# Performance work log

Hardware: AMD Instinct MI355X
Metric: run time of the kernel (lower is better)

Reference implementation:

```python
import jax, jax.numpy as jnp
import numpy as np

B, T, HID = 8, 1024, 2048
H, D = 16, 128          # num_attention_heads, head_dim (num_kv_heads = 1)
Q_RANK, KV_RANK = 128, 64
EPS = 1e-6
MIN_VAL = -1e9          # fp32 branch of create_causal_padding_mask


def _rmsnorm(x, w, eps=EPS):
    return x * jax.lax.rsqrt(jnp.mean(x * x, axis=-1, keepdims=True) + eps) * w


def _rope(x, cos, sin):
    x1, x2 = jnp.split(x, 2, axis=-1)
    return jnp.concatenate([x1 * cos - x2 * sin, x2 * cos + x1 * sin], axis=-1)


def setup_inputs() -> dict:
    key = jax.random.key(0)
    ks = jax.random.split(key, 12)
    s = lambda fan_in: 1.0 / np.sqrt(fan_in)
    return {
        'hidden_states': jax.random.normal(ks[0], (B, T, HID), jnp.float32),
        'cos_g': jax.random.uniform(ks[1], (1, T, 1, D // 2), jnp.float32, -1.0, 1.0),
        'sin_g': jax.random.uniform(ks[2], (1, T, 1, D // 2), jnp.float32, -1.0, 1.0),
        'cos_l': jax.random.uniform(ks[3], (1, T, 1, D // 2), jnp.float32, -1.0, 1.0),
        'sin_l': jax.random.uniform(ks[4], (1, T, 1, D // 2), jnp.float32, -1.0, 1.0),
        'Wq_a': jax.random.normal(ks[5], (HID, Q_RANK), jnp.float32) * s(HID),
        'bq_a': jnp.zeros((Q_RANK,), jnp.float32),
        'Wq_b': jax.random.normal(ks[6], (Q_RANK, H * D), jnp.float32) * s(Q_RANK),
        'bq_b': jnp.zeros((H * D,), jnp.float32),
        'Wkv_a': jax.random.normal(ks[7], (HID, KV_RANK), jnp.float32) * s(HID),
        'bkv_a': jnp.zeros((KV_RANK,), jnp.float32),
        'Wkv_b': jax.random.normal(ks[8], (KV_RANK, 2 * D), jnp.float32) * s(KV_RANK),
        'bkv_b': jnp.zeros((2 * D,), jnp.float32),
        'q_norm_w': jnp.ones((D,), jnp.float32),
        'kv_norm_w': jnp.ones((KV_RANK,), jnp.float32),
        'Wo': jax.random.normal(ks[9], (H * D, HID), jnp.float32) * s(H * D),
        'nope_logit': jnp.array([-2.0], jnp.float32),
        'gl_logit': jnp.array([np.log(0.01 / 0.99)], jnp.float32),
        'attention_mask': jnp.ones((B, T), jnp.int32),
    }


def reference(hidden_states, cos_g, sin_g, cos_l, sin_l,
              Wq_a, bq_a, Wq_b, bq_b, Wkv_a, bkv_a, Wkv_b, bkv_b,
              q_norm_w, kv_norm_w, Wo, nope_logit, gl_logit, attention_mask):
    h = hidden_states
    # learned global/local RoPE blend
    a = jax.nn.sigmoid(gl_logit).reshape(1, 1, 1, 1)
    cos = cos_g * a + cos_l * (1.0 - a)
    sin = sin_g * a + sin_l * (1.0 - a)

    # LoRA q path: q_b(RMSNorm(q_a(h)))
    q = _rmsnorm(h @ Wq_a + bq_a, q_norm_w) @ Wq_b + bq_b      # [B,T,H*D]
    q = q.reshape(B, T, H, D)
    q_pe = _rope(q, cos, sin)

    # LoRA kv path: kv_b(RMSNorm(kv_a(h)))  (single kv head)
    kv = _rmsnorm(h @ Wkv_a + bkv_a, kv_norm_w) @ Wkv_b + bkv_b  # [B,T,2*D]
    k, v = jnp.split(kv, 2, axis=-1)                            # [B,T,D] each
    k_pe = _rope(k.reshape(B, T, 1, D), cos, sin)[:, :, 0, :]   # [B,T,D]

    # nope/rope alpha mix
    na = jax.nn.sigmoid(nope_logit).reshape(1, 1, 1, 1)
    q_f = na * q + (1.0 - na) * q_pe                            # [B,T,H,D]
    k_f = na[..., 0] * k + (1.0 - na[..., 0]) * k_pe            # [B,T,D]

    # causal + padding additive mask
    causal = jnp.triu(jnp.ones((T, T), bool), k=1)              # [T,T]
    pad = (attention_mask == 0)[:, None, None, :]               # [B,1,1,T]
    add_mask = jnp.where(causal[None, None] | pad, MIN_VAL, 0.0).astype(h.dtype)

    scale = D ** -0.5
    scores = jnp.einsum('bthd,bsd->bhts', q_f, k_f) * scale + add_mask
    attn = jax.nn.softmax(scores, axis=-1)                      # [B,H,T,T]
    out = jnp.einsum('bhts,bsd->bthd', attn, v)                 # [B,T,H,D]
    return out.reshape(B, T, H * D) @ Wo
```

## Files before the change

### kernel.cpp

```cpp
#include <hip/hip_runtime.h>
#include <hip/hip_bf16.h>

typedef __attribute__((ext_vector_type(8))) short bf16x8;
typedef __attribute__((ext_vector_type(4))) float f32x4;
typedef __attribute__((ext_vector_type(4))) unsigned short us4;

#define DEV __device__ __forceinline__

constexpr int Bc = 8, Tc = 1024, HIDc = 2048, Hc = 16, Dc = 128;
constexpr int ROWSc = Bc * Tc;

DEV unsigned short f2bfb(float x) {
  union { float f; unsigned u; } v; v.f = x;
  unsigned r = v.u + 0x7fffu + ((v.u >> 16) & 1u);
  return (unsigned short)(r >> 16);
}
DEV float bfb2f(unsigned short b) {
  union { unsigned u; float f; } v; v.u = ((unsigned)b) << 16; return v.f;
}
DEV float fexp2(float x) { return __builtin_amdgcn_exp2f(x); }
DEV unsigned pkbf(float lo, float hi) {
  union { float f; unsigned u; } a, b; a.f = lo; b.f = hi;
  return ((b.u + 0x8000u) & 0xffff0000u) | ((a.u + 0x8000u) >> 16);
}

DEV void gload16(const void* g, void* l) {
  __builtin_amdgcn_global_load_lds(
      (const __attribute__((address_space(1))) unsigned int*)g,
      (__attribute__((address_space(3))) unsigned int*)l, 16, 0, 0);
}


__global__ void k_blend(const float* __restrict__ cg, const float* __restrict__ sg,
                        const float* __restrict__ cl, const float* __restrict__ sl,
                        const float* __restrict__ gl,
                        float* __restrict__ cosb, float* __restrict__ sinb) {
  int u = blockIdx.x * 256 + threadIdx.x;
  if (u >= Tc * 64) return;
  float a = 1.0f / (1.0f + __expf(-gl[0]));
  cosb[u] = cg[u] * a + cl[u] * (1.0f - a);
  sinb[u] = sg[u] * a + sl[u] * (1.0f - a);
}

__global__ void k_zero(unsigned short* __restrict__ p, int n) {
  int i = blockIdx.x * 256 + threadIdx.x;
  if (i < n) p[i] = 0;
}

__global__ __launch_bounds__(256) void k_transpose(const float* __restrict__ in,
                                                   unsigned short* __restrict__ out,
                                                   int R, int C) {
  __shared__ float tile[32][33];
  int tx = threadIdx.x & 31, ty = threadIdx.x >> 5;
  int r0 = blockIdx.y * 32, c0 = blockIdx.x * 32;
#pragma unroll
  for (int i = 0; i < 4; i++)
    tile[ty + i * 8][tx] = in[(size_t)(r0 + ty + i * 8) * C + c0 + tx];
  __syncthreads();
#pragma unroll
  for (int i = 0; i < 4; i++) {
    int rr = ty + i * 8;
    out[(size_t)(c0 + rr) * R + r0 + tx] = f2bfb(tile[tx][rr]);
  }
}


__global__ __launch_bounds__(256) void k_gemm1(const float* __restrict__ A,
                                               const unsigned short* __restrict__ Bt,
                                               float* __restrict__ C) {
  constexpr int K = 2048, N = 256;
  __shared__ __align__(16) unsigned short As[64 * 32];
  __shared__ __align__(16) unsigned short Bs[128 * 32];
  int lin = blockIdx.x;
  int wg = (lin & 7) * 32 + (lin >> 3);
  int m0 = (wg >> 1) * 64, n0 = (wg & 1) * 128;
  int tid = threadIdx.x, lane = tid & 63, wc = tid >> 6;
  int ar = tid >> 2, akc = (tid & 3) * 8;
  const float* Ag = A + (size_t)(m0 + ar) * K + akc;
  const unsigned short* Bg0 = Bt + (size_t)(n0 + ar) * K + akc;
  const unsigned short* Bg1 = Bt + (size_t)(n0 + 64 + ar) * K + akc;
  unsigned short* Bsl0 = &Bs[tid * 8];
  unsigned short* Bsl1 = &Bs[2048 + tid * 8];
  f32x4 acc[4][2];
  f32x4 zz = {0.f, 0.f, 0.f, 0.f};
#pragma unroll
  for (int m = 0; m < 4; m++)
#pragma unroll
    for (int n = 0; n < 2; n++) acc[m][n] = zz;
  int fr = lane & 15, fk = (lane >> 4) * 8;
  for (int kt = 0; kt < K; kt += 32) {
    float4 a0 = *(const float4*)(Ag + kt);
    float4 a1 = *(const float4*)(Ag + kt + 4);
    __syncthreads();
    gload16(Bg0 + kt, Bsl0);
    gload16(Bg1 + kt, Bsl1);
    us4 c0 = { f2bfb(a0.x), f2bfb(a0.y), f2bfb(a0.z), f2bfb(a0.w) };
    us4 c1 = { f2bfb(a1.x), f2bfb(a1.y), f2bfb(a1.z), f2bfb(a1.w) };
    *(us4*)&As[ar * 32 + akc] = c0;
    *(us4*)&As[ar * 32 + akc + 4] = c1;
    __syncthreads();
    bf16x8 af[4], bfv[2];
#pragma unroll
    for (int i = 0; i < 4; i++)
      af[i] = *(const bf16x8*)&As[(i * 16 + fr) * 32 + fk];
#pragma unroll
    for (int i = 0; i < 2; i++)
      bfv[i] = *(const bf16x8*)&Bs[(wc * 32 + i * 16 + fr) * 32 + fk];
    __builtin_amdgcn_s_setprio(1);
#pragma unroll
    for (int m = 0; m < 4; m++)
#pragma unroll
      for (int n = 0; n < 2; n++)
        acc[m][n] = __builtin_amdgcn_mfma_f32_16x16x32_bf16(af[m], bfv[n], acc[m][n], 0, 0, 0);
    __builtin_amdgcn_s_setprio(0);
  }
  int gg = lane >> 4;
#pragma unroll
  for (int m = 0; m < 4; m++)
#pragma unroll
    for (int n = 0; n < 2; n++)
#pragma unroll
      for (int r = 0; r < 4; r++) {
        size_t row = (size_t)m0 + m * 16 + gg * 4 + r;
        size_t col = (size_t)n0 + wc * 32 + n * 16 + fr;
        C[row * N + col] = acc[m][n][r];
      }
}


template <int OUTB>
__global__ __launch_bounds__(256) void k_gemm(const unsigned short* __restrict__ A,
                                              const unsigned short* __restrict__ Bt,
                                              void* __restrict__ outp,
                                              int M, int N, int K, int nx) {
  __shared__ __align__(16) unsigned short As[4096];
  __shared__ __align__(16) unsigned short Bs[4096];
  int lin = blockIdx.x;
  int qq = gridDim.x >> 3;
  int wg = (lin & 7) * qq + (lin >> 3);
  int m0 = (wg / nx) * 128, n0 = (wg % nx) * 128;
  int tid = threadIdx.x;
  int lane = tid & 63;
  int wave = tid >> 6;
  int wr = wave >> 1, wc = wave & 1;
  int srow = tid >> 2;
  int skc = (tid & 3) * 8;
  const unsigned short* Ag0 = A + (size_t)(m0 + srow) * K + skc;
  const unsigned short* Ag1 = A + (size_t)(m0 + 64 + srow) * K + skc;
  const unsigned short* Bg0 = Bt + (size_t)(n0 + srow) * K + skc;
  const unsigned short* Bg1 = Bt + (size_t)(n0 + 64 + srow) * K + skc;
  unsigned short* Asl0 = &As[tid * 8];
  unsigned short* Asl1 = &As[2048 + tid * 8];
  unsigned short* Bsl0 = &Bs[tid * 8];
  unsigned short* Bsl1 = &Bs[2048 + tid * 8];
  f32x4 acc[4][4];
  f32x4 zz = {0.f, 0.f, 0.f, 0.f};
#pragma unroll
  for (int m = 0; m < 4; m++)
#pragma unroll
    for (int n = 0; n < 4; n++) acc[m][n] = zz;
  int fr = lane & 15, fk = (lane >> 4) * 8;
  for (int kt = 0; kt < K; kt += 32) {
    __syncthreads();
    gload16(Ag0 + kt, Asl0);
    gload16(Ag1 + kt, Asl1);
    gload16(Bg0 + kt, Bsl0);
    gload16(Bg1 + kt, Bsl1);
    __syncthreads();
    bf16x8 af[4], bfv[4];
#pragma unroll
    for (int i = 0; i < 4; i++)
      af[i] = *(const bf16x8*)&As[(wr * 64 + i * 16 + fr) * 32 + fk];
#pragma unroll
    for (int i = 0; i < 4; i++)
      bfv[i] = *(const bf16x8*)&Bs[(wc * 64 + i * 16 + fr) * 32 + fk];
    __builtin_amdgcn_s_setprio(1);
#pragma unroll
    for (int m = 0; m < 4; m++)
#pragma unroll
      for (int n = 0; n < 4; n++)
        acc[m][n] = __builtin_amdgcn_mfma_f32_16x16x32_bf16(af[m], bfv[n], acc[m][n], 0, 0, 0);
    __builtin_amdgcn_s_setprio(0);
  }
  int gg = lane >> 4;
#pragma unroll
  for (int m = 0; m < 4; m++)
#pragma unroll
    for (int n = 0; n < 4; n++)
#pragma unroll
      for (int r = 0; r < 4; r++) {
        size_t row = (size_t)m0 + wr * 64 + m * 16 + gg * 4 + r;
        size_t col = (size_t)n0 + wc * 64 + n * 16 + fr;
        if (OUTB)
          ((unsigned short*)outp)[row * N + col] = f2bfb(acc[m][n][r]);
        else
          ((float*)outp)[row * N + col] = acc[m][n][r];
      }
}


__global__ __launch_bounds__(512, 2) void k_gemm3(const unsigned short* __restrict__ A,
                                                  const unsigned short* __restrict__ Bt,
                                                  float* __restrict__ C) {
  constexpr int K = 2048, N = 2048, NT = K / 64;
  __shared__ __align__(16) unsigned short Als[2][2][8192];
  __shared__ __align__(16) unsigned short Bls[2][2][8192];
  int lin = blockIdx.x;
  int wg = (lin & 7) * 32 + (lin >> 3);
  int m0 = (wg >> 3) * 256, n0 = (wg & 7) * 256;
  int tid = threadIdx.x, lane = tid & 63, wave = tid >> 6;
  int wm = wave >> 2, wn = wave & 3;
  int g = lane >> 4, c = lane & 15;

  int rb = tid >> 2;
  int sch = (tid & 3) ^ ((tid >> 3) & 3);
  const unsigned short* Ag = A + (size_t)(m0 + rb) * K + sch * 8;
  const unsigned short* Bg = Bt + (size_t)(n0 + rb) * K + sch * 8;
  const int gsw = (g ^ ((c >> 1) & 3)) * 8;

  f32x4 acc[8][4];
  f32x4 zz = {0.f, 0.f, 0.f, 0.f};
#pragma unroll
  for (int mi = 0; mi < 8; mi++)
#pragma unroll
    for (int ni = 0; ni < 4; ni++) acc[mi][ni] = zz;

#pragma unroll
  for (int sl = 0; sl < 2; sl++) {
    gload16(Ag + sl * 32, &Als[0][sl][tid * 8]);
    gload16(Ag + (size_t)128 * K + sl * 32, &Als[0][sl][4096 + tid * 8]);
    gload16(Bg + sl * 32, &Bls[0][sl][tid * 8]);
    gload16(Bg + (size_t)128 * K + sl * 32, &Bls[0][sl][4096 + tid * 8]);
  }

  for (int t = 0; t < NT; ++t) {
    int buf = t & 1, nb = buf ^ 1;
    bool nl = (t + 1 < NT);
    int nkt = (t + 1) * 64;
#pragma unroll
    for (int sl = 0; sl < 2; sl++) {
      if (sl == 0 || nl) {
        asm volatile("s_waitcnt vmcnt(4)" ::: "memory");
      } else {
        asm volatile("s_waitcnt vmcnt(0)" ::: "memory");
      }
      __builtin_amdgcn_sched_barrier(0);
      __builtin_amdgcn_s_barrier();
      __builtin_amdgcn_sched_barrier(0);
      const unsigned short* As_ = &Als[buf][sl][0];
      const unsigned short* Bs_ = &Bls[buf][sl][0];
      bf16x8 af[8], bfv[4];
#pragma unroll
      for (int mi = 0; mi < 8; mi++)
        af[mi] = *(const bf16x8*)&As_[(wm * 128 + mi * 16 + c) * 32 + gsw];
#pragma unroll
      for (int ni = 0; ni < 4; ni++)
        bfv[ni] = *(const bf16x8*)&Bs_[(wn * 64 + ni * 16 + c) * 32 + gsw];
      if (nl) {
        gload16(Ag + nkt + sl * 32, &Als[nb][sl][tid * 8]);
        gload16(Ag + (size_t)128 * K + nkt + sl * 32, &Als[nb][sl][4096 + tid * 8]);
      }
      __builtin_amdgcn_s_setprio(1);
#pragma unroll
      for (int mi = 0; mi < 8; mi++) {
        acc[mi][0] = __builtin_amdgcn_mfma_f32_16x16x32_bf16(af[mi], bfv[0], acc[mi][0], 0, 0, 0);
        acc[mi][1] = __builtin_amdgcn_mfma_f32_16x16x32_bf16(af[mi], bfv[1], acc[mi][1], 0, 0, 0);
      }
      __builtin_amdgcn_s_setprio(0);
      if (nl) {
        gload16(Bg + nkt + sl * 32, &Bls[nb][sl][tid * 8]);
        gload16(Bg + (size_t)128 * K + nkt + sl * 32, &Bls[nb][sl][4096 + tid * 8]);
      }
      __builtin_amdgcn_s_setprio(1);
#pragma unroll
      for (int mi = 0; mi < 8; mi++) {
        acc[mi][2] = __builtin_amdgcn_mfma_f32_16x16x32_bf16(af[mi], bfv[2], acc[mi][2], 0, 0, 0);
        acc[mi][3] = __builtin_amdgcn_mfma_f32_16x16x32_bf16(af[mi], bfv[3], acc[mi][3], 0, 0, 0);
      }
      __builtin_amdgcn_s_setprio(0);
    }
  }

#pragma unroll
  for (int mi = 0; mi < 8; mi++)
#pragma unroll
    for (int ni = 0; ni < 4; ni++)
#pragma unroll
      for (int r = 0; r < 4; r++) {
        size_t row = (size_t)m0 + wm * 128 + mi * 16 + g * 4 + r;
        size_t col = (size_t)n0 + wn * 64 + ni * 16 + c;
        C[row * N + col] = acc[mi][ni][r];
      }
}


__global__ __launch_bounds__(256) void k_gemm2q(const unsigned short* __restrict__ A,
                                                const unsigned short* __restrict__ Bt,
                                                const float* __restrict__ bqb,
                                                const float* __restrict__ cosb,
                                                const float* __restrict__ sinb,
                                                const float* __restrict__ nl,
                                                unsigned short* __restrict__ Qf) {
  constexpr int K = 128, N = 2048;
  __shared__ __align__(16) unsigned short As[4096];
  __shared__ __align__(16) unsigned short Bs[4096];
  __shared__ __align__(16) unsigned short Qt[128 * 128];
  int lin = blockIdx.x;
  int wg = (lin & 7) * 128 + (lin >> 3);
  int m0 = (wg >> 4) * 128, n0 = (wg & 15) * 128;
  int h = n0 >> 7;
  int b = m0 >> 10, t0 = m0 & 1023;
  int tid = threadIdx.x;
  int lane = tid & 63;
  int wave = tid >> 6;
  int wr = wave >> 1, wc = wave & 1;
  int srow = tid >> 2;
  int skc = (tid & 3) * 8;
  const unsigned short* Ag0 = A + (size_t)(m0 + srow) * K + skc;
  const unsigned short* Ag1 = A + (size_t)(m0 + 64 + srow) * K + skc;
  const unsigned short* Bg0 = Bt + (size_t)(n0 + srow) * K + skc;
  const unsigned short* Bg1 = Bt + (size_t)(n0 + 64 + srow) * K + skc;
  unsigned short* Asl0 = &As[tid * 8];
  unsigned short* Asl1 = &As[2048 + tid * 8];
  unsigned short* Bsl0 = &Bs[tid * 8];
  unsigned short* Bsl1 = &Bs[2048 + tid * 8];
  f32x4 acc[4][4];
  f32x4 zz = {0.f, 0.f, 0.f, 0.f};
#pragma unroll
  for (int m = 0; m < 4; m++)
#pragma unroll
    for (int n = 0; n < 4; n++) acc[m][n] = zz;
  int fr = lane & 15, fk = (lane >> 4) * 8;
  for (int kt = 0; kt < K; kt += 32) {
    __syncthreads();
    gload16(Ag0 + kt, Asl0);
    gload16(Ag1 + kt, Asl1);
    gload16(Bg0 + kt, Bsl0);
    gload16(Bg1 + kt, Bsl1);
    __syncthreads();
    bf16x8 af[4], bfv[4];
#pragma unroll
    for (int i = 0; i < 4; i++)
      af[i] = *(const bf16x8*)&As[(wr * 64 + i * 16 + fr) * 32 + fk];
#pragma unroll
    for (int i = 0; i < 4; i++)
      bfv[i] = *(const bf16x8*)&Bs[(wc * 64 + i * 16 + fr) * 32 + fk];
    __builtin_amdgcn_s_setprio(1);
#pragma unroll
    for (int m = 0; m < 4; m++)
#pragma unroll
      for (int n = 0; n < 4; n++)
        acc[m][n] = __builtin_amdgcn_mfma_f32_16x16x32_bf16(af[m], bfv[n], acc[m][n], 0, 0, 0);
    __builtin_amdgcn_s_setprio(0);
  }
  int gg = lane >> 4;
#pragma unroll
  for (int n = 0; n < 4; n++) {
    int col = wc * 64 + n * 16 + fr;
    float bias = bqb[h * 128 + col];
    int ch = col >> 3, wi = col & 7;
#pragma unroll
    for (int m = 0; m < 4; m++)
#pragma unroll
      for (int r = 0; r < 4; r++) {
        int lrow = wr * 64 + m * 16 + gg * 4 + r;
        Qt[lrow * 128 + ((ch ^ (lrow & 7)) << 3) + wi] = f2bfb(acc[m][n][r] + bias);
      }
  }
  __syncthreads();
  const float SCLQ = 0.08838834764831845f * 1.4426950408889634f;
  float na = 1.0f / (1.0f + __expf(-nl[0]));
  float nb = 1.0f - na;
#pragma unroll
  for (int it = 0; it < 4; it++) {
    int task = it * 256 + tid;
    int lrow = task >> 3, cp = task & 7;
    int t = t0 + lrow;
    bf16x8 v1 = *(const bf16x8*)&Qt[lrow * 128 + ((cp ^ (lrow & 7)) << 3)];
    bf16x8 v2 = *(const bf16x8*)&Qt[lrow * 128 + (((cp + 8) ^ (lrow & 7)) << 3)];
    float4 cA = *(const float4*)(cosb + t * 64 + cp * 8);
    float4 cB = *(const float4*)(cosb + t * 64 + cp * 8 + 4);
    float4 sA = *(const float4*)(sinb + t * 64 + cp * 8);
    float4 sB = *(const float4*)(sinb + t * 64 + cp * 8 + 4);
    float cv[8] = {cA.x, cA.y, cA.z, cA.w, cB.x, cB.y, cB.z, cB.w};
    float sv[8] = {sA.x, sA.y, sA.z, sA.w, sB.x, sB.y, sB.z, sB.w};
    float f1[8], f2[8];
#pragma unroll
    for (int j = 0; j < 8; j++) {
      float q1 = bfb2f((unsigned short)v1[j]);
      float q2 = bfb2f((unsigned short)v2[j]);
      float p1 = q1 * cv[j] - q2 * sv[j];
      float p2 = q2 * cv[j] + q1 * sv[j];
      f1[j] = (na * q1 + nb * p1) * SCLQ;
      f2[j] = (na * q2 + nb * p2) * SCLQ;
    }
    unsigned short* ob = Qf + ((size_t)(b * Hc + h) * Tc + t) * Dc + cp * 8;
    us4 o0 = {f2bfb(f1[0]), f2bfb(f1[1]), f2bfb(f1[2]), f2bfb(f1[3])};
    us4 o1 = {f2bfb(f1[4]), f2bfb(f1[5]), f2bfb(f1[6]), f2bfb(f1[7])};
    us4 o2 = {f2bfb(f2[0]), f2bfb(f2[1]), f2bfb(f2[2]), f2bfb(f2[3])};
    us4 o3 = {f2bfb(f2[4]), f2bfb(f2[5]), f2bfb(f2[6]), f2bfb(f2[7])};
    *(us4*)(ob) = o0;
    *(us4*)(ob + 4) = o1;
    *(us4*)(ob + 64) = o2;
    *(us4*)(ob + 68) = o3;
  }
}


__global__ __launch_bounds__(256) void k_norm(const float* __restrict__ A1,
                                              const float* __restrict__ bqa,
                                              const float* __restrict__ bkva,
                                              const float* __restrict__ qw,
                                              const float* __restrict__ kvw,
                                              unsigned short* __restrict__ Qn,
                                              unsigned short* __restrict__ Kvn) {
  int wave = threadIdx.x >> 6, lane = threadIdx.x & 63;
  int row = blockIdx.x * 4 + wave;
  const float* a = A1 + (size_t)row * 256;
  float x0 = a[lane] + bqa[lane];
  float x1 = a[64 + lane] + bqa[64 + lane];
  float ss = x0 * x0 + x1 * x1;
#pragma unroll
  for (int off = 1; off < 64; off <<= 1) ss += __shfl_xor(ss, off);
  float sc = rsqrtf(ss * (1.0f / 128.0f) + 1e-6f);
  Qn[(size_t)row * 128 + lane] = f2bfb(x0 * sc * qw[lane]);
  Qn[(size_t)row * 128 + 64 + lane] = f2bfb(x1 * sc * qw[64 + lane]);
  float y = a[128 + lane] + bkva[lane];
  float s2 = y * y;
#pragma unroll
  for (int off = 1; off < 64; off <<= 1) s2 += __shfl_xor(s2, off);
  float sc2 = rsqrtf(s2 * (1.0f / 64.0f) + 1e-6f);
  Kvn[(size_t)row * 64 + lane] = f2bfb(y * sc2 * kvw[lane]);
}


__global__ __launch_bounds__(256) void k_rope_kv(const unsigned short* __restrict__ kvr,
                                                 const float* __restrict__ bkvb,
                                                 const float* __restrict__ cosb,
                                                 const float* __restrict__ sinb,
                                                 const float* __restrict__ nl,
                                                 unsigned short* __restrict__ Kf,
                                                 unsigned short* __restrict__ Vt) {
  int u = blockIdx.x * 256 + threadIdx.x;
  int row = u >> 6, d = u & 63;
  int t = row & (Tc - 1), b = row >> 10;
  float na = 1.0f / (1.0f + __expf(-nl[0]));
  const unsigned short* kp = kvr + (size_t)row * 256;
  float k1 = bfb2f(kp[d]) + bkvb[d];
  float k2 = bfb2f(kp[64 + d]) + bkvb[64 + d];
  float v1 = bfb2f(kp[128 + d]) + bkvb[128 + d];
  float v2 = bfb2f(kp[192 + d]) + bkvb[192 + d];
  float cv = cosb[t * 64 + d], sv = sinb[t * 64 + d];
  float p1 = k1 * cv - k2 * sv;
  float p2 = k2 * cv + k1 * sv;
  float f1 = na * k1 + (1.0f - na) * p1;
  float f2 = na * k2 + (1.0f - na) * p2;
  unsigned short* kb = Kf + (size_t)row * Dc;
  kb[d] = f2bfb(f1);
  kb[64 + d] = f2bfb(f2);
  Vt[((size_t)b * Dc + d) * Tc + t] = f2bfb(v1);
  Vt[((size_t)b * Dc + 64 + d) * Tc + t] = f2bfb(v2);
}


__global__ __launch_bounds__(512, 1) void k_attn(const unsigned short* __restrict__ Qf,
                                                 const unsigned short* __restrict__ Kf,
                                                 const unsigned short* __restrict__ Vt,
                                                 const int* __restrict__ amask,
                                                 unsigned short* __restrict__ O) {
  __shared__ __align__(16) unsigned short Ks[2][64 * 128];
  __shared__ __align__(16) unsigned short Vs[2][128 * 64];
  __shared__ __align__(16) unsigned short Plds[8][32 * 64];
  __shared__ int s_anyzero;

  int bid = blockIdx.x;
  int b = bid & 7;
  int pr = (bid >> 3) & 1;
  int h = bid >> 4;
  int tid = threadIdx.x;
  int wave = tid >> 6, lane = tid & 63;
  int g = lane >> 4, c = lane & 15;

  const unsigned short* Kp = Kf + (size_t)b * Tc * Dc;
  const unsigned short* Vp = Vt + (size_t)b * Dc * Tc;
  const int* mp = amask + b * Tc;
  char* PwB = (char*)&Plds[wave][0];
  f32x4 zz = {0.f, 0.f, 0.f, 0.f};

  if (tid == 0) s_anyzero = 0;
  __syncthreads();
  if (mp[tid] == 0 || mp[tid + 512] == 0) s_anyzero = 1;
  __syncthreads();
  bool anyz = (s_anyzero != 0);

  int kr_ = tid >> 3, kc_ = tid & 7;
  int vr_ = tid >> 2, vc_ = tid & 3;
  int kidx0 = kr_ * 128 + ((kc_ ^ (kr_ & 7)) << 3);
  int kidx1 = kr_ * 128 + (((kc_ + 8) ^ (kr_ & 7)) << 3);
  int vidx0 = vr_ * 64 + ((vc_ ^ (vr_ & 7)) << 3);
  int vidx1 = vr_ * 64 + (((vc_ + 4) ^ (vr_ & 7)) << 3);

  int c7s = (c & 7) << 4;
  int g4 = g * 4;

  for (int pass = 0; pass < 2; pass++) {
    int sp = (pass == 0) ? pr : 3 - pr;
    int qw0 = sp * 256 + wave * 32;
    int nt = (sp + 1) * 4;
    const unsigned short* Qp = Qf + ((size_t)(b * Hc + h) * Tc + qw0) * Dc;
    bf16x8 qfr[2][4];
#pragma unroll
    for (int m = 0; m < 2; m++)
#pragma unroll
      for (int ks = 0; ks < 4; ks++)
        qfr[m][ks] = *(const bf16x8*)(Qp + (size_t)(m * 16 + c) * Dc + ks * 32 + g * 8);

    f32x4 Oacc[2][8];
#pragma unroll
    for (int m = 0; m < 2; m++)
#pragma unroll
      for (int i = 0; i < 8; i++) Oacc[m][i] = zz;
    float m_r[2] = {-1e30f, -1e30f};
    float l_r[2] = {0.f, 0.f};

    bf16x8 krg[2], vrg[2];
    krg[0] = *(const bf16x8*)(Kp + (size_t)kr_ * Dc + kc_ * 8);
    krg[1] = *(const bf16x8*)(Kp + (size_t)kr_ * Dc + kc_ * 8 + 64);
    vrg[0] = *(const bf16x8*)(Vp + (size_t)vr_ * Tc + vc_ * 8);
    vrg[1] = *(const bf16x8*)(Vp + (size_t)vr_ * Tc + vc_ * 8 + 32);
    __syncthreads();
    *(bf16x8*)&Ks[0][kidx0] = krg[0];
    *(bf16x8*)&Ks[0][kidx1] = krg[1];
    *(bf16x8*)&Vs[0][vidx0] = vrg[0];
    *(bf16x8*)&Vs[0][vidx1] = vrg[1];
    __syncthreads();

    for (int st = 0; st < nt; st++) {
      int cur = st & 1;
      int s0 = st << 6;
      if (st + 1 < nt) {
        int s1 = s0 + 64;
        krg[0] = *(const bf16x8*)(Kp + (size_t)(s1 + kr_) * Dc + kc_ * 8);
        krg[1] = *(const bf16x8*)(Kp + (size_t)(s1 + kr_) * Dc + kc_ * 8 + 64);
        vrg[0] = *(const bf16x8*)(Vp + (size_t)vr_ * Tc + s1 + vc_ * 8);
        vrg[1] = *(const bf16x8*)(Vp + (size_t)vr_ * Tc + s1 + vc_ * 8 + 32);
      }

      if (s0 <= qw0 + 31) {
        const unsigned short* Kc = &Ks[cur][0];
        const unsigned short* Vc = &Vs[cur][0];

        f32x4 S[2][4];
#pragma unroll
        for (int m = 0; m < 2; m++)
#pragma unroll
          for (int j = 0; j < 4; j++) S[m][j] = zz;
        __builtin_amdgcn_s_setprio(1);
#pragma unroll
        for (int ks = 0; ks < 4; ks++)
#pragma unroll
          for (int j = 0; j < 4; j++) {
            bf16x8 kfr = *(const bf16x8*)&Kc[(j * 16 + c) * 128 + (((ks * 4 + g) ^ (c & 7)) << 3)];
            S[0][j] = __builtin_amdgcn_mfma_f32_16x16x32_bf16(kfr, qfr[0][ks], S[0][j], 0, 0, 0);
            S[1][j] = __builtin_amdgcn_mfma_f32_16x16x32_bf16(kfr, qfr[1][ks], S[1][j], 0, 0, 0);
          }
        __builtin_amdgcn_s_setprio(0);

        if (anyz) {
#pragma unroll
          for (int j = 0; j < 4; j++)
#pragma unroll
            for (int r = 0; r < 4; r++) {
              float madd = (mp[s0 + j * 16 + g4 + r] == 0) ? -2e9f : 0.0f;
              S[0][j][r] += madd;
              S[1][j][r] += madd;
            }
        }
        if (s0 + 63 > qw0) {
#pragma unroll
          for (int j = 0; j < 4; j++) {
            int kk = s0 + j * 16 + g4;
#pragma unroll
            for (int r = 0; r < 4; r++) {
#pragma unroll
              for (int m = 0; m < 2; m++)
                if (kk + r > qw0 + m * 16 + c) S[m][j][r] = -1e30f;
            }
          }
        }

        float tmax[2];
#pragma unroll
        for (int m = 0; m < 2; m++) {
          float t0 = fmaxf(fmaxf(S[m][0][0], S[m][0][1]), fmaxf(S[m][0][2], S[m][0][3]));
          float t1 = fmaxf(fmaxf(S[m][1][0], S[m][1][1]), fmaxf(S[m][1][2], S[m][1][3]));
          float t2 = fmaxf(fmaxf(S[m][2][0], S[m][2][1]), fmaxf(S[m][2][2], S[m][2][3]));
          float t3 = fmaxf(fmaxf(S[m][3][0], S[m][3][1]), fmaxf(S[m][3][2], S[m][3][3]));
          float t = fmaxf(fmaxf(t0, t1), fmaxf(t2, t3));
          t = fmaxf(t, __shfl_xor(t, 16));
          t = fmaxf(t, __shfl_xor(t, 32));
          tmax[m] = t;
        }
        bool upd = (tmax[0] > m_r[0] + 11.0f) || (tmax[1] > m_r[1] + 11.0f);
        if (__any(upd)) {
#pragma unroll
          for (int m = 0; m < 2; m++) {
            float mn = fmaxf(m_r[m], tmax[m]);
            float al = fexp2(m_r[m] - mn);
            m_r[m] = mn;
            l_r[m] *= al;
#pragma unroll
            for (int r = 0; r < 4; r++) {
              float alr = __shfl(al, (lane & 48) | (g4 + r));
#pragma unroll
              for (int j2 = 0; j2 < 8; j2++) Oacc[m][j2][r] *= alr;
            }
          }
        }

#pragma unroll
        for (int m = 0; m < 2; m++) {
          int rowb = (m * 16 + c) * 128;
#pragma unroll
          for (int j = 0; j < 4; j++) {
            float e0 = fexp2(S[m][j][0] - m_r[m]);
            float e1 = fexp2(S[m][j][1] - m_r[m]);
            float e2 = fexp2(S[m][j][2] - m_r[m]);
            float e3 = fexp2(S[m][j][3] - m_r[m]);
            l_r[m] += (e0 + e1) + (e2 + e3);
            uint2 w;
            w.x = pkbf(e0, e1);
            w.y = pkbf(e2, e3);
            int inrow = (j * 32 + g * 8) ^ c7s;
            *(uint2*)(PwB + rowb + inrow) = w;
          }
        }

        asm volatile("s_waitcnt lgkmcnt(0)" ::: "memory");
        bf16x8 pa[2][2];
#pragma unroll
        for (int m = 0; m < 2; m++)
#pragma unroll
          for (int sk = 0; sk < 2; sk++)
            pa[m][sk] = *(const bf16x8*)(PwB + (m * 16 + c) * 128 + (((sk * 64 + g * 16)) ^ c7s));
        __builtin_amdgcn_s_setprio(1);
#pragma unroll
        for (int sk = 0; sk < 2; sk++)
#pragma unroll
          for (int j2 = 0; j2 < 8; j2++) {
            int row = j2 * 16 + c;
            bf16x8 vfr = *(const bf16x8*)&Vc[row * 64 + (((sk * 4 + g) ^ (row & 7)) << 3)];
            Oacc[0][j2] = __builtin_amdgcn_mfma_f32_16x16x32_bf16(pa[0][sk], vfr, Oacc[0][j2], 0, 0, 0);
            Oacc[1][j2] = __builtin_amdgcn_mfma_f32_16x16x32_bf16(pa[1][sk], vfr, Oacc[1][j2], 0, 0, 0);
          }
        __builtin_amdgcn_s_setprio(0);
      }

      if (st + 1 < nt) {
        int nxt = cur ^ 1;
        *(bf16x8*)&Ks[nxt][kidx0] = krg[0];
        *(bf16x8*)&Ks[nxt][kidx1] = krg[1];
        *(bf16x8*)&Vs[nxt][vidx0] = vrg[0];
        *(bf16x8*)&Vs[nxt][vidx1] = vrg[1];
      }
      __syncthreads();
    }

#pragma unroll
    for (int m = 0; m < 2; m++) {
      float lt = l_r[m];
      lt += __shfl_xor(lt, 16);
      lt += __shfl_xor(lt, 32);
      float inv = 1.0f / lt;
#pragma unroll
      for (int r = 0; r < 4; r++) {
        float invr = __shfl(inv, (lane & 48) | (g4 + r));
        int qr = qw0 + m * 16 + g4 + r;
        unsigned short* ob = O + ((size_t)(b * Tc) + qr) * HIDc + h * Dc;
#pragma unroll
        for (int j2 = 0; j2 < 8; j2++) ob[j2 * 16 + c] = f2bfb(Oacc[m][j2][r] * invr);
      }
    }
  }
}


extern "C" void kernel_launch(void* const* d_in, const int* in_sizes, int n_in,
                              void* d_out, int out_size, void* d_ws, size_t ws_size,
                              hipStream_t stream) {
  const float* h = (const float*)d_in[0];
  const float* cg = (const float*)d_in[1];
  const float* sg = (const float*)d_in[2];
  const float* cl = (const float*)d_in[3];
  const float* sl = (const float*)d_in[4];
  const float* Wq_a = (const float*)d_in[5];
  const float* bq_a = (const float*)d_in[6];
  const float* Wq_b = (const float*)d_in[7];
  const float* bq_b = (const float*)d_in[8];
  const float* Wkv_a = (const float*)d_in[9];
  const float* bkv_a = (const float*)d_in[10];
  const float* Wkv_b = (const float*)d_in[11];
  const float* bkv_b = (const float*)d_in[12];
  const float* qw = (const float*)d_in[13];
  const float* kvw = (const float*)d_in[14];
  const float* Wo = (const float*)d_in[15];
  const float* nl = (const float*)d_in[16];
  const float* gl = (const float*)d_in[17];
  const int* am = (const int*)d_in[18];
  float* out = (float*)d_out;
  char* ws = (char*)d_ws;

  const size_t o_hB = 0;
  const size_t o_Qf = 67108864;
  const size_t o_A1 = 100663296;
  const size_t o_Qn = 109051904;
  const size_t o_Kvn = 111149056;
  const size_t o_kvr = 112197632;
  const size_t o_Kf = 116391936;
  const size_t o_Vt = 118489088;
  const size_t o_W1t = 120586240;
  const size_t o_Wqbt = 121634816;
  const size_t o_Wkbt = 122159104;
  const size_t o_Wot = 122191872;
  const size_t o_cos = 130580480;
  const size_t o_sin = 130842624;

  unsigned short* Obuf = (unsigned short*)(ws + o_hB);
  unsigned short* Qf = (unsigned short*)(ws + o_Qf);
  float* A1 = (float*)(ws + o_A1);
  unsigned short* Qn = (unsigned short*)(ws + o_Qn);
  unsigned short* Kvn = (unsigned short*)(ws + o_Kvn);
  unsigned short* kvr = (unsigned short*)(ws + o_kvr);
  unsigned short* Kf = (unsigned short*)(ws + o_Kf);
  unsigned short* Vt = (unsigned short*)(ws + o_Vt);
  unsigned short* W1t = (unsigned short*)(ws + o_W1t);
  unsigned short* Wqbt = (unsigned short*)(ws + o_Wqbt);
  unsigned short* Wkbt = (unsigned short*)(ws + o_Wkbt);
  unsigned short* Wot = (unsigned short*)(ws + o_Wot);
  float* cosb = (float*)(ws + o_cos);
  float* sinb = (float*)(ws + o_sin);

  (void)in_sizes; (void)n_in; (void)out_size; (void)ws_size;

  k_blend<<<256, 256, 0, stream>>>(cg, sg, cl, sl, gl, cosb, sinb);
  k_zero<<<512, 256, 0, stream>>>(W1t + (size_t)192 * 2048, 64 * 2048);
  k_transpose<<<dim3(4, 64), 256, 0, stream>>>(Wq_a, W1t, 2048, 128);
  k_transpose<<<dim3(2, 64), 256, 0, stream>>>(Wkv_a, W1t + (size_t)128 * 2048, 2048, 64);
  k_transpose<<<dim3(64, 4), 256, 0, stream>>>(Wq_b, Wqbt, 128, 2048);
  k_transpose<<<dim3(8, 2), 256, 0, stream>>>(Wkv_b, Wkbt, 64, 256);
  k_transpose<<<dim3(64, 64), 256, 0, stream>>>(Wo, Wot, 2048, 2048);

  k_gemm1<<<256, 256, 0, stream>>>(h, W1t, A1);
  k_norm<<<2048, 256, 0, stream>>>(A1, bq_a, bkv_a, qw, kvw, Qn, Kvn);
  k_gemm2q<<<1024, 256, 0, stream>>>(Qn, Wqbt, bq_b, cosb, sinb, nl, Qf);
  k_gemm<1><<<128, 256, 0, stream>>>(Kvn, Wkbt, kvr, ROWSc, 256, 64, 2);
  k_rope_kv<<<2048, 256, 0, stream>>>(kvr, bkv_b, cosb, sinb, nl, Kf, Vt);
  k_attn<<<256, 512, 0, stream>>>(Qf, Kf, Vt, am, Obuf);
  k_gemm3<<<256, 512, 0, stream>>>(Obuf, Wot, out);
}
```

Baseline: 226.7 us.

## Split-K the first LoRA GEMM and double-buffer its LDS tiles

The first down-projection GEMM (hidden to the q/kv LoRA ranks) is split along K into two halves, doubling the grid from 256 to 512 workgroups so the MI355X's CUs are better occupied. Each half writes its own partial fp32 output, and the norm kernel sums the two partials before RMSNorm. The main loop is also software-pipelined with double-buffered LDS, so global loads for the next tile overlap MFMA work on the current one. The cost is an extra 8 MB partial buffer to write and read, plus twice the LDS per block.

```diff
diff --git a/kernel.cpp b/kernel.cpp
--- a/kernel.cpp
+++ b/kernel.cpp
@@ -67,20 +67,23 @@
 
 __global__ __launch_bounds__(256) void k_gemm1(const float* __restrict__ A,
                                                const unsigned short* __restrict__ Bt,
-                                               float* __restrict__ C) {
-  constexpr int K = 2048, N = 256;
-  __shared__ __align__(16) unsigned short As[64 * 32];
-  __shared__ __align__(16) unsigned short Bs[128 * 32];
+                                               float* __restrict__ C0,
+                                               float* __restrict__ C1) {
+  constexpr int K = 2048, N = 256, KH = 1024, NT = KH / 32;
+  __shared__ __align__(16) unsigned short Als[2][64 * 32];
+  __shared__ __align__(16) unsigned short Bls[2][128 * 32];
   int lin = blockIdx.x;
-  int wg = (lin & 7) * 32 + (lin >> 3);
-  int m0 = (wg >> 1) * 64, n0 = (wg & 1) * 128;
+  int wg = (lin & 7) * 64 + (lin >> 3);
+  int ksl = wg & 1;
+  int nti = (wg >> 1) & 1;
+  int mti = wg >> 2;
+  int m0 = mti * 64, n0 = nti * 128, k0 = ksl * KH;
+  float* C = ksl ? C1 : C0;
   int tid = threadIdx.x, lane = tid & 63, wc = tid >> 6;
   int ar = tid >> 2, akc = (tid & 3) * 8;
-  const float* Ag = A + (size_t)(m0 + ar) * K + akc;
-  const unsigned short* Bg0 = Bt + (size_t)(n0 + ar) * K + akc;
-  const unsigned short* Bg1 = Bt + (size_t)(n0 + 64 + ar) * K + akc;
-  unsigned short* Bsl0 = &Bs[tid * 8];
-  unsigned short* Bsl1 = &Bs[2048 + tid * 8];
+  const float* Ag = A + (size_t)(m0 + ar) * K + k0 + akc;
+  const unsigned short* Bg0 = Bt + (size_t)(n0 + ar) * K + k0 + akc;
+  const unsigned short* Bg1 = Bt + (size_t)(n0 + 64 + ar) * K + k0 + akc;
   f32x4 acc[4][2];
   f32x4 zz = {0.f, 0.f, 0.f, 0.f};
 #pragma unroll
@@ -88,24 +91,34 @@
 #pragma unroll
     for (int n = 0; n < 2; n++) acc[m][n] = zz;
   int fr = lane & 15, fk = (lane >> 4) * 8;
-  for (int kt = 0; kt < K; kt += 32) {
-    float4 a0 = *(const float4*)(Ag + kt);
-    float4 a1 = *(const float4*)(Ag + kt + 4);
-    __syncthreads();
-    gload16(Bg0 + kt, Bsl0);
-    gload16(Bg1 + kt, Bsl1);
-    us4 c0 = { f2bfb(a0.x), f2bfb(a0.y), f2bfb(a0.z), f2bfb(a0.w) };
-    us4 c1 = { f2bfb(a1.x), f2bfb(a1.y), f2bfb(a1.z), f2bfb(a1.w) };
-    *(us4*)&As[ar * 32 + akc] = c0;
-    *(us4*)&As[ar * 32 + akc + 4] = c1;
-    __syncthreads();
+
+  float4 a0 = *(const float4*)(Ag);
+  float4 a1 = *(const float4*)(Ag + 4);
+  gload16(Bg0, &Bls[0][tid * 8]);
+  gload16(Bg1, &Bls[0][2048 + tid * 8]);
+  {
+    us4 c0v = { f2bfb(a0.x), f2bfb(a0.y), f2bfb(a0.z), f2bfb(a0.w) };
+    us4 c1v = { f2bfb(a1.x), f2bfb(a1.y), f2bfb(a1.z), f2bfb(a1.w) };
+    *(us4*)&Als[0][ar * 32 + akc] = c0v;
+    *(us4*)&Als[0][ar * 32 + akc + 4] = c1v;
+  }
+  a0 = *(const float4*)(Ag + 32);
+  a1 = *(const float4*)(Ag + 36);
+  __syncthreads();
+
+  for (int t = 0; t < NT; t++) {
+    int cur = t & 1, nxt = cur ^ 1;
+    if (t + 1 < NT) {
+      gload16(Bg0 + (t + 1) * 32, &Bls[nxt][tid * 8]);
+      gload16(Bg1 + (t + 1) * 32, &Bls[nxt][2048 + tid * 8]);
+    }
     bf16x8 af[4], bfv[2];
 #pragma unroll
     for (int i = 0; i < 4; i++)
-      af[i] = *(const bf16x8*)&As[(i * 16 + fr) * 32 + fk];
+      af[i] = *(const bf16x8*)&Als[cur][(i * 16 + fr) * 32 + fk];
 #pragma unroll
     for (int i = 0; i < 2; i++)
-      bfv[i] = *(const bf16x8*)&Bs[(wc * 32 + i * 16 + fr) * 32 + fk];
+      bfv[i] = *(const bf16x8*)&Bls[cur][(wc * 32 + i * 16 + fr) * 32 + fk];
     __builtin_amdgcn_s_setprio(1);
 #pragma unroll
     for (int m = 0; m < 4; m++)
@@ -113,6 +126,17 @@
       for (int n = 0; n < 2; n++)
         acc[m][n] = __builtin_amdgcn_mfma_f32_16x16x32_bf16(af[m], bfv[n], acc[m][n], 0, 0, 0);
     __builtin_amdgcn_s_setprio(0);
+    if (t + 1 < NT) {
+      us4 d0 = { f2bfb(a0.x), f2bfb(a0.y), f2bfb(a0.z), f2bfb(a0.w) };
+      us4 d1 = { f2bfb(a1.x), f2bfb(a1.y), f2bfb(a1.z), f2bfb(a1.w) };
+      *(us4*)&Als[nxt][ar * 32 + akc] = d0;
+      *(us4*)&Als[nxt][ar * 32 + akc + 4] = d1;
+    }
+    if (t + 2 < NT) {
+      a0 = *(const float4*)(Ag + (t + 2) * 32);
+      a1 = *(const float4*)(Ag + (t + 2) * 32 + 4);
+    }
+    __syncthreads();
   }
   int gg = lane >> 4;
 #pragma unroll
@@ -408,6 +432,7 @@
 
 
 __global__ __launch_bounds__(256) void k_norm(const float* __restrict__ A1,
+                                              const float* __restrict__ A1b,
                                               const float* __restrict__ bqa,
                                               const float* __restrict__ bkva,
                                               const float* __restrict__ qw,
@@ -417,15 +442,16 @@
   int wave = threadIdx.x >> 6, lane = threadIdx.x & 63;
   int row = blockIdx.x * 4 + wave;
   const float* a = A1 + (size_t)row * 256;
-  float x0 = a[lane] + bqa[lane];
-  float x1 = a[64 + lane] + bqa[64 + lane];
+  const float* a2 = A1b + (size_t)row * 256;
+  float x0 = a[lane] + a2[lane] + bqa[lane];
+  float x1 = a[64 + lane] + a2[64 + lane] + bqa[64 + lane];
   float ss = x0 * x0 + x1 * x1;
 #pragma unroll
   for (int off = 1; off < 64; off <<= 1) ss += __shfl_xor(ss, off);
   float sc = rsqrtf(ss * (1.0f / 128.0f) + 1e-6f);
   Qn[(size_t)row * 128 + lane] = f2bfb(x0 * sc * qw[lane]);
   Qn[(size_t)row * 128 + 64 + lane] = f2bfb(x1 * sc * qw[64 + lane]);
-  float y = a[128 + lane] + bkva[lane];
+  float y = a[128 + lane] + a2[128 + lane] + bkva[lane];
   float s2 = y * y;
 #pragma unroll
   for (int off = 1; off < 64; off <<= 1) s2 += __shfl_xor(s2, off);
@@ -711,6 +737,7 @@
   char* ws = (char*)d_ws;
 
   const size_t o_hB = 0;
+  const size_t o_A1b = 33554432;
   const size_t o_Qf = 67108864;
   const size_t o_A1 = 100663296;
   const size_t o_Qn = 109051904;
@@ -726,6 +753,7 @@
   const size_t o_sin = 130842624;
 
   unsigned short* Obuf = (unsigned short*)(ws + o_hB);
+  float* A1b = (float*)(ws + o_A1b);
   unsigned short* Qf = (unsigned short*)(ws + o_Qf);
   float* A1 = (float*)(ws + o_A1);
   unsigned short* Qn = (unsigned short*)(ws + o_Qn);
@@ -750,8 +778,8 @@
   k_transpose<<<dim3(8, 2), 256, 0, stream>>>(Wkv_b, Wkbt, 64, 256);
   k_transpose<<<dim3(64, 64), 256, 0, stream>>>(Wo, Wot, 2048, 2048);
 
-  k_gemm1<<<256, 256, 0, stream>>>(h, W1t, A1);
-  k_norm<<<2048, 256, 0, stream>>>(A1, bq_a, bkv_a, qw, kvw, Qn, Kvn);
+  k_gemm1<<<512, 256, 0, stream>>>(h, W1t, A1, A1b);
+  k_norm<<<2048, 256, 0, stream>>>(A1, A1b, bq_a, bkv_a, qw, kvw, Qn, Kvn);
   k_gemm2q<<<1024, 256, 0, stream>>>(Qn, Wqbt, bq_b, cosb, sinb, nl, Qf);
   k_gemm<1><<<128, 256, 0, stream>>>(Kvn, Wkbt, kvr, ROWSc, 256, 64, 2);
   k_rope_kv<<<2048, 256, 0, stream>>>(kvr, bkv_b, cosb, sinb, nl, Kf, Vt);
```

Measured after the change: 216.3 us. -4.6%, faster.
